# Kernel optimization log

Hardware: AMD Instinct MI355X
Metric: run time of the kernel (lower is better)

Reference implementation:

```python
import jax, jax.numpy as jnp
import numpy as np

DIM = 512
NUM_HEAD = 8
HEAD_DIM = DIM // NUM_HEAD
FFN = 4 * DIM


def setup_inputs() -> dict:
    key = jax.random.key(0)
    ks = jax.random.split(key, 16)
    s = DIM ** -0.5
    inp = {
        "x": jax.random.normal(ks[0], (4, 2048, DIM), jnp.float32),
        "wq": jax.random.normal(ks[1], (DIM, DIM), jnp.float32) * s,
        "bq": jnp.zeros((DIM,), jnp.float32),
        "wk": jax.random.normal(ks[2], (DIM, DIM), jnp.float32) * s,
        "bk": jnp.zeros((DIM,), jnp.float32),
        "wv": jax.random.normal(ks[3], (DIM, DIM), jnp.float32) * s,
        "bv": jnp.zeros((DIM,), jnp.float32),
        "wo": jax.random.normal(ks[4], (DIM, DIM), jnp.float32) * s,
        "bo": jnp.zeros((DIM,), jnp.float32),
        "w1": jax.random.normal(ks[5], (DIM, FFN), jnp.float32) * s,
        "b1": jnp.zeros((FFN,), jnp.float32),
        "w2": jax.random.normal(ks[6], (FFN, DIM), jnp.float32) * (FFN ** -0.5),
        "b2": jnp.zeros((DIM,), jnp.float32),
        "g1": jnp.ones((DIM,), jnp.float32),
        "be1": jnp.zeros((DIM,), jnp.float32),
        "g2": jnp.ones((DIM,), jnp.float32),
        "be2": jnp.zeros((DIM,), jnp.float32),
    }
    return inp


def layer_norm(x, g, b, eps=1e-5):
    mu = jnp.mean(x, axis=-1, keepdims=True)
    var = jnp.var(x, axis=-1, keepdims=True)
    return (x - mu) * jax.lax.rsqrt(var + eps) * g + b


def _forward(x, wq, bq, wk, bk, wv, bv, wo, bo, w1, b1, w2, b2, g1, be1, g2, be2):
    b, n, _ = x.shape
    scale = HEAD_DIM ** -0.5
    q = (x @ wq + bq).reshape(b, n, NUM_HEAD, HEAD_DIM).transpose(0, 2, 1, 3)
    k = (x @ wk + bk).reshape(b, n, NUM_HEAD, HEAD_DIM).transpose(0, 2, 1, 3)
    v = (x @ wv + bv).reshape(b, n, NUM_HEAD, HEAD_DIM).transpose(0, 2, 1, 3)
    scores = jnp.einsum('bhqd,bhkd->bhqk', q, k) * scale
    attn = jax.nn.softmax(scores, axis=-1)
    out = jnp.einsum('bhqk,bhkd->bhqd', attn, v)
    out = out.transpose(0, 2, 1, 3).reshape(b, n, DIM)
    out = out @ wo + bo
    x = layer_norm(out + x, g1, be1)
    h = jax.nn.gelu(x @ w1 + b1, approximate=False)
    ff = h @ w2 + b2
    x = layer_norm(ff + x, g2, be2)
    return x


def reference(x, wq, bq, wk, bk, wv, bv, wo, bo, w1, b1, w2, b2, g1, be1, g2, be2):
    return _forward(x, wq, bq, wk, bk, wv, bv, wo, bo, w1, b1, w2, b2, g1, be1, g2, be2)
```

## Files before the change

kernel.cpp:

```cpp
#include <hip/hip_runtime.h>
#include <math.h>

#define DIM 512
#define NHEAD 8
#define HD 64
#define FFN_DIM 2048
#define BATCH 4
#define SEQ 2048
#define MTOK (BATCH*SEQ)

typedef __attribute__((ext_vector_type(8))) short bf16x8;
typedef __attribute__((ext_vector_type(4))) short bf16x4;
typedef __attribute__((ext_vector_type(4))) float f32x4;
typedef __attribute__((ext_vector_type(2))) unsigned int u32x2;
typedef __attribute__((ext_vector_type(4))) unsigned int u32x4;

__device__ __forceinline__ unsigned short f2b(float f){
    unsigned int u = __float_as_uint(f);
    u += 0x7fffu + ((u >> 16) & 1u);
    return (unsigned short)(u >> 16);
}
__device__ __forceinline__ float b2f(unsigned short u){
    return __uint_as_float(((unsigned int)u) << 16);
}
__device__ __forceinline__ unsigned int pack_trunc(float f0, float f1){
    return __builtin_amdgcn_perm(__float_as_uint(f1), __float_as_uint(f0), 0x07060302u);
}
__device__ __forceinline__ void async_cp16(const unsigned short* g, unsigned short* l){
    __builtin_amdgcn_global_load_lds((const __attribute__((address_space(1))) unsigned int*)g,
                                     (__attribute__((address_space(3))) unsigned int*)l, 16, 0, 0);
}
__device__ __forceinline__ float gelu_fast(float x){
    float x3 = x*x*x;
    float y  = 2.302588f * (x + 0.044715f*x3);
    float t  = __builtin_amdgcn_exp2f(y);
    return x * t * __builtin_amdgcn_rcpf(t + 1.0f);
}

__device__ __forceinline__ void transp32(const float* __restrict__ in, unsigned short* __restrict__ out,
                                         int N, int K, int n0_rd, int n0_wr, int k0,
                                         unsigned short (&t)[32][33], int tid){
    int tx = tid & 31, ty = tid >> 5;
    #pragma unroll
    for (int u = 0; u < 4; u++)
        t[tx][ty + 8*u] = f2b(in[(size_t)(k0 + ty + 8*u)*N + n0_rd + tx]);
    __syncthreads();
    #pragma unroll
    for (int u = 0; u < 4; u++)
        out[(size_t)(n0_wr + ty + 8*u)*K + k0 + tx] = t[ty + 8*u][tx];
}

__global__ void prep_kernel(const float* __restrict__ x,
                            const float* __restrict__ wq, const float* __restrict__ wk,
                            const float* __restrict__ wv, const float* __restrict__ wo,
                            const float* __restrict__ w1, const float* __restrict__ w2,
                            const float* __restrict__ bq, const float* __restrict__ bk,
                            const float* __restrict__ bv,
                            unsigned short* __restrict__ xb, unsigned short* __restrict__ wqkvT,
                            unsigned short* __restrict__ woT, unsigned short* __restrict__ w1T,
                            unsigned short* __restrict__ w2T, float* __restrict__ bqkv)
{
    __shared__ unsigned short t[32][33];
    int bid = blockIdx.x, tid = threadIdx.x;
    if (bid < 4096) {
        int i = (bid*256 + tid)*4;
        float4 v = *(const float4*)(x + i);
        ushort4 o; o.x=f2b(v.x); o.y=f2b(v.y); o.z=f2b(v.z); o.w=f2b(v.w);
        *(ushort4*)(xb + i) = o;
    } else if (bid < 4864) {
        int r = bid - 4096;
        int n0 = (r % 48)*32, k0 = (r / 48)*32;
        const float* w = (n0 < 512) ? wq : (n0 < 1024) ? wk : wv;
        transp32(w, wqkvT, 512, 512, n0 & 511, n0, k0, t, tid);
    } else if (bid < 5120) {
        int r = bid - 4864;
        int n0 = (r % 16)*32, k0 = (r / 16)*32;
        transp32(wo, woT, 512, 512, n0, n0, k0, t, tid);
    } else if (bid < 6144) {
        int r = bid - 5120;
        int n0 = (r % 64)*32, k0 = (r / 64)*32;
        transp32(w1, w1T, 2048, 512, n0, n0, k0, t, tid);
    } else if (bid < 7168) {
        int r = bid - 6144;
        int n0 = (r % 16)*32, k0 = (r / 16)*32;
        transp32(w2, w2T, 512, 2048, n0, n0, k0, t, tid);
    } else {
        int i = (bid - 7168)*256 + tid;
        if (i < 1536)
            bqkv[i] = (i < 512) ? bq[i] : (i < 1024) ? bk[i-512] : bv[i-1024];
    }
}

template<int MODE, int SK>
__global__ __launch_bounds__(256, 4)
void gemm_bf16(const unsigned short* __restrict__ A, const unsigned short* __restrict__ Bt,
               const float* __restrict__ bias,
               unsigned short* __restrict__ Cb,
               unsigned short* __restrict__ qo, unsigned short* __restrict__ ko,
               unsigned short* __restrict__ vTo,
               int M, int N, int K)
{
    __shared__ unsigned short As[128*64];
    __shared__ unsigned short Bs[128*64];
    int tid  = threadIdx.x;
    int lane = tid & 63;
    int ln = lane & 15, qd = lane >> 4;
    int m0 = blockIdx.x * 128, n0 = blockIdx.y * 128;
    int wid = tid >> 6;
    int wm = (wid >> 1) * 64;
    int wn = (wid & 1) * 64;
    int kbeg = (SK > 1) ? (int)blockIdx.z * (K/SK) : 0;
    int kend = kbeg + K/SK;
    if (SK > 1 && MODE == 0) Cb += (size_t)blockIdx.z * M * N;

    f32x4 acc[4][4];
    #pragma unroll
    for (int i = 0; i < 4; i++)
        #pragma unroll
        for (int j = 0; j < 4; j++) acc[i][j] = (f32x4){0.f,0.f,0.f,0.f};

    for (int k0 = kbeg; k0 < kend; k0 += 64) {
        #pragma unroll
        for (int i = 0; i < 4; i++) {
            int cid = i*256 + tid;
            int row = cid >> 3, cs = cid & 7;
            int cg = cs ^ (row & 7);
            async_cp16(&A[(size_t)(m0+row)*K + k0 + cg*8], &As[(cid & ~63) * 8]);
        }
        #pragma unroll
        for (int i = 0; i < 4; i++) {
            int cid = i*256 + tid;
            int row = cid >> 3, cs = cid & 7;
            int cg = cs ^ (row & 7);
            async_cp16(&Bt[(size_t)(n0+row)*K + k0 + cg*8], &Bs[(cid & ~63) * 8]);
        }
        __syncthreads();
        #pragma unroll
        for (int kk = 0; kk < 64; kk += 32) {
            int c0 = kk >> 3;
            bf16x8 af[4], bf[4];
            #pragma unroll
            for (int t = 0; t < 4; t++)
                af[t] = *(bf16x8*)&As[(wm + t*16 + ln)*64 + ((c0 + qd) ^ (ln & 7))*8];
            #pragma unroll
            for (int t = 0; t < 4; t++)
                bf[t] = *(bf16x8*)&Bs[(wn + t*16 + ln)*64 + ((c0 + qd) ^ (ln & 7))*8];
            #pragma unroll
            for (int i = 0; i < 4; i++)
                #pragma unroll
                for (int j = 0; j < 4; j++)
                    acc[i][j] = __builtin_amdgcn_mfma_f32_16x16x32_bf16(af[i], bf[j], acc[i][j], 0,0,0);
        }
        __syncthreads();
    }

    const float QSCALE = 0.18033688011112042f;
    #pragma unroll
    for (int i = 0; i < 4; i++) {
        int mb = m0 + wm + i*16 + qd*4;
        #pragma unroll
        for (int j = 0; j < 4; j++) {
            int c = n0 + wn + j*16 + ln;
            float bv_ = (SK > 1 && blockIdx.z) ? 0.f : bias[c];
            float v[4];
            #pragma unroll
            for (int r = 0; r < 4; r++) v[r] = acc[i][j][r] + bv_;
            if (MODE == 0) {
                #pragma unroll
                for (int r = 0; r < 4; r++) Cb[(size_t)(mb+r)*N + c] = f2b(v[r]);
            } else if (MODE == 2) {
                #pragma unroll
                for (int r = 0; r < 4; r++)
                    Cb[(size_t)(mb+r)*N + c] = f2b(gelu_fast(v[r]));
            } else {
                int b = mb >> 11, t0 = mb & 2047;
                if (c < 512) {
                    int h = c >> 6, hd = c & 63;
                    #pragma unroll
                    for (int r = 0; r < 4; r++)
                        qo[(((size_t)(b*8 + h))*SEQ + t0 + r)*64 + hd] = f2b(v[r] * QSCALE);
                } else if (c < 1024) {
                    int cc = c - 512, h = cc >> 6, hd = cc & 63;
                    #pragma unroll
                    for (int r = 0; r < 4; r++)
                        ko[(((size_t)(b*8 + h))*SEQ + t0 + r)*64 + hd] = f2b(v[r]);
                } else {
                    int cc = c - 1024, h = cc >> 6, hd = cc & 63;
                    ushort4 pk;
                    pk.x = f2b(v[0]); pk.y = f2b(v[1]); pk.z = f2b(v[2]); pk.w = f2b(v[3]);
                    *(ushort4*)&vTo[(((size_t)(b*8 + h))*64 + hd)*SEQ + t0] = pk;
                }
            }
        }
    }
}

#define ATTN_BODY(KT_, KOF_, PREF_, VMC_)                                               \
  {                                                                                     \
    asm volatile("s_waitcnt vmcnt(" #VMC_ ")" ::: "memory");                            \
    __builtin_amdgcn_s_barrier();                                                       \
    __builtin_amdgcn_sched_barrier(0);                                                  \
    if (PREF_) {                                                                        \
      const int nb = (KOF_ + 16384) % 24576;                                            \
      async_cp16(&K [((size_t)bh*SEQ + ((KT_)+2)*64 + srow)*64 + scg*8], &lds[nb + sdst]); \
      async_cp16(&VT[((size_t)bh*64 + srow)*SEQ + ((KT_)+2)*64 + scg*8], &lds[nb + 4096 + sdst]); \
    }                                                                                   \
    bf16x8 kf[2][2];                                                                    \
    _Pragma("unroll")                                                                   \
    for (int ntl = 0; ntl < 2; ntl++) {                                                 \
      kf[ntl][0] = *(const bf16x8*)&kp0[(KOF_) + ntl*1024];                             \
      kf[ntl][1] = *(const bf16x8*)&kp1[(KOF_) + ntl*1024];                             \
    }                                                                                   \
    f32x4 s[2][2];                                                                      \
    _Pragma("unroll")                                                                   \
    for (int qs = 0; qs < 2; qs++)                                                      \
      _Pragma("unroll")                                                                 \
      for (int ntl = 0; ntl < 2; ntl++) s[qs][ntl] = (f32x4){0.f,0.f,0.f,0.f};          \
    __builtin_amdgcn_s_setprio(1);                                                      \
    _Pragma("unroll")                                                                   \
    for (int kk = 0; kk < 2; kk++) {                                                    \
      _Pragma("unroll")                                                                 \
      for (int ntl = 0; ntl < 2; ntl++) {                                               \
        s[0][ntl] = __builtin_amdgcn_mfma_f32_16x16x32_bf16(kf[ntl][kk], qf[0][kk], s[0][ntl], 0,0,0); \
        s[1][ntl] = __builtin_amdgcn_mfma_f32_16x16x32_bf16(kf[ntl][kk], qf[1][kk], s[1][ntl], 0,0,0); \
      }                                                                                 \
    }                                                                                   \
    __builtin_amdgcn_s_setprio(0);                                                      \
    bf16x8 pf[2];                                                                       \
    _Pragma("unroll")                                                                   \
    for (int qs = 0; qs < 2; qs++) {                                                    \
      float p[8];                                                                       \
      _Pragma("unroll")                                                                 \
      for (int ntl = 0; ntl < 2; ntl++)                                                 \
        _Pragma("unroll")                                                               \
        for (int r = 0; r < 4; r++) p[ntl*4+r] = __builtin_amdgcn_exp2f(s[qs][ntl][r]); \
      l_i[qs] += ((p[0]+p[1])+(p[2]+p[3])) + ((p[4]+p[5])+(p[6]+p[7]));                 \
      u32x4 pu;                                                                         \
      pu[0] = pack_trunc(p[0], p[1]); pu[1] = pack_trunc(p[2], p[3]);                   \
      pu[2] = pack_trunc(p[4], p[5]); pu[3] = pack_trunc(p[6], p[7]);                   \
      pf[qs] = __builtin_bit_cast(bf16x8, pu);                                          \
    }                                                                                   \
    __builtin_amdgcn_s_setprio(1);                                                      \
    _Pragma("unroll")                                                                   \
    for (int dt = 0; dt < 4; dt++) {                                                    \
      u32x2 va = *(const u32x2*)&vpA[(KOF_) + 4096 + dt*1024];                          \
      u32x2 vb = *(const u32x2*)&vpB[(KOF_) + 4096 + dt*1024];                          \
      u32x4 vv; vv[0] = va[0]; vv[1] = va[1]; vv[2] = vb[0]; vv[3] = vb[1];             \
      bf16x8 vf = __builtin_bit_cast(bf16x8, vv);                                       \
      o[0][dt] = __builtin_amdgcn_mfma_f32_16x16x32_bf16(vf, pf[0], o[0][dt], 0,0,0);   \
      o[1][dt] = __builtin_amdgcn_mfma_f32_16x16x32_bf16(vf, pf[1], o[1][dt], 0,0,0);   \
    }                                                                                   \
    __builtin_amdgcn_s_setprio(0);                                                      \
  }

__global__ __launch_bounds__(512, 2)
void attn_mfma(const unsigned short* __restrict__ Q, const unsigned short* __restrict__ K,
               const unsigned short* __restrict__ VT, unsigned short* __restrict__ O)
{
    __shared__ unsigned short lds[24576];
    int tid  = threadIdx.x;
    int wid  = tid >> 6, lane = tid & 63;
    int ln = lane & 15, qd = lane >> 4;
    int wq = wid & 3;
    int wk = wid >> 2;
    int bx = blockIdx.x;
    int qb = (bx >> 3) & 15;
    int bh = (bx & 7) + 8 * (bx >> 7);

    bf16x8 qf[2][2];
    #pragma unroll
    for (int qs = 0; qs < 2; qs++)
        #pragma unroll
        for (int kk = 0; kk < 2; kk++)
            qf[qs][kk] = *(const bf16x8*)&Q[((size_t)bh*SEQ + qb*128 + wq*32 + qs*16 + ln)*64 + kk*32 + qd*8];

    int srow = tid >> 3, scs = tid & 7, scg = scs ^ (srow & 7);
    int sdst = (tid & ~63) * 8;
    #pragma unroll
    for (int t = 0; t < 2; t++) {
        async_cp16(&K [((size_t)bh*SEQ + t*64 + srow)*64 + scg*8], &lds[t*8192 + sdst]);
        async_cp16(&VT[((size_t)bh*64 + srow)*SEQ + t*64 + scg*8], &lds[t*8192 + 4096 + sdst]);
    }

    const unsigned short* kp0 = lds + wk*2048 + ln*64 + ((0*4 + qd) ^ (ln & 7))*8;
    const unsigned short* kp1 = lds + wk*2048 + ln*64 + ((1*4 + qd) ^ (ln & 7))*8;
    const unsigned short* vpA = lds + ln*64 + ((wk*4     + (qd>>1)) ^ (ln & 7))*8 + (qd & 1)*4;
    const unsigned short* vpB = lds + ln*64 + ((wk*4 + 2 + (qd>>1)) ^ (ln & 7))*8 + (qd & 1)*4;

    f32x4 o[2][4];
    #pragma unroll
    for (int qs = 0; qs < 2; qs++)
        #pragma unroll
        for (int dt = 0; dt < 4; dt++) o[qs][dt] = (f32x4){0.f,0.f,0.f,0.f};
    float l_i[2] = {0.f, 0.f};

    for (int kt3 = 0; kt3 < 30; kt3 += 3) {
        ATTN_BODY(kt3 + 0, 0,     true, 2)
        ATTN_BODY(kt3 + 1, 8192,  true, 2)
        ATTN_BODY(kt3 + 2, 16384, true, 2)
    }
    ATTN_BODY(30, 0,    false, 2)
    ATTN_BODY(31, 8192, false, 0)

    float l[2];
    #pragma unroll
    for (int qs = 0; qs < 2; qs++) {
        float t = l_i[qs];
        t += __shfl_xor(t, 16);
        t += __shfl_xor(t, 32);
        l[qs] = t;
    }

    __syncthreads();
    float* fl = (float*)lds;
    if (wk == 1) {
        #pragma unroll
        for (int qs = 0; qs < 2; qs++) {
            #pragma unroll
            for (int dt = 0; dt < 4; dt++)
                *(f32x4*)&fl[(((wq*2 + qs)*4 + dt)*64 + lane)*4] = o[qs][dt];
            fl[8192 + (wq*2 + qs)*64 + lane] = l[qs];
        }
    }
    __syncthreads();
    if (wk == 0) {
        int b = bh >> 3, h = bh & 7;
        #pragma unroll
        for (int qs = 0; qs < 2; qs++) {
            float lt = l[qs] + fl[8192 + (wq*2 + qs)*64 + lane];
            float linv = 1.0f / lt;
            int t = qb*128 + wq*32 + qs*16 + ln;
            #pragma unroll
            for (int dt = 0; dt < 4; dt++) {
                f32x4 po = *(f32x4*)&fl[(((wq*2 + qs)*4 + dt)*64 + lane)*4];
                ushort4 pk;
                pk.x = f2b((o[qs][dt][0] + po[0])*linv);
                pk.y = f2b((o[qs][dt][1] + po[1])*linv);
                pk.z = f2b((o[qs][dt][2] + po[2])*linv);
                pk.w = f2b((o[qs][dt][3] + po[3])*linv);
                *(ushort4*)&O[((size_t)b*SEQ + t)*DIM + h*64 + dt*16 + qd*4] = pk;
            }
        }
    }
}

__global__ void ln1_kernel(const unsigned short* __restrict__ m0b, const unsigned short* __restrict__ m1b,
                           const float* __restrict__ resp,
                           const float* __restrict__ g, const float* __restrict__ be,
                           unsigned short* __restrict__ outb)
{
    int row  = blockIdx.x*4 + (threadIdx.x >> 6);
    int lane = threadIdx.x & 63;
    size_t base = (size_t)row * DIM + lane*8;

    ushort4 a0 = *(const ushort4*)(m0b + base);
    ushort4 a1 = *(const ushort4*)(m0b + base + 4);
    ushort4 c0 = *(const ushort4*)(m1b + base);
    ushort4 c1 = *(const ushort4*)(m1b + base + 4);
    float4 r0 = *(const float4*)(resp + base);
    float4 r1 = *(const float4*)(resp + base + 4);
    float v[8] = { b2f(a0.x)+b2f(c0.x)+r0.x, b2f(a0.y)+b2f(c0.y)+r0.y,
                   b2f(a0.z)+b2f(c0.z)+r0.z, b2f(a0.w)+b2f(c0.w)+r0.w,
                   b2f(a1.x)+b2f(c1.x)+r1.x, b2f(a1.y)+b2f(c1.y)+r1.y,
                   b2f(a1.z)+b2f(c1.z)+r1.z, b2f(a1.w)+b2f(c1.w)+r1.w };
    float s = 0.f, s2 = 0.f;
    #pragma unroll
    for (int i = 0; i < 8; i++) { s += v[i]; s2 += v[i]*v[i]; }
    #pragma unroll
    for (int d = 32; d >= 1; d >>= 1) { s += __shfl_xor(s, d); s2 += __shfl_xor(s2, d); }
    float mean = s * (1.0f / DIM);
    float rstd = rsqrtf(s2 * (1.0f / DIM) - mean*mean + 1e-5f);

    float4 g0 = *(const float4*)(g + lane*8);
    float4 g1 = *(const float4*)(g + lane*8 + 4);
    float4 b0 = *(const float4*)(be + lane*8);
    float4 b1 = *(const float4*)(be + lane*8 + 4);
    float gg[8] = {g0.x,g0.y,g0.z,g0.w,g1.x,g1.y,g1.z,g1.w};
    float bb[8] = {b0.x,b0.y,b0.z,b0.w,b1.x,b1.y,b1.z,b1.w};
    float o[8];
    #pragma unroll
    for (int i = 0; i < 8; i++) o[i] = (v[i]-mean)*rstd*gg[i] + bb[i];
    ushort4 p0, p1;
    p0.x=f2b(o[0]); p0.y=f2b(o[1]); p0.z=f2b(o[2]); p0.w=f2b(o[3]);
    p1.x=f2b(o[4]); p1.y=f2b(o[5]); p1.z=f2b(o[6]); p1.w=f2b(o[7]);
    *(ushort4*)(outb + base)     = p0;
    *(ushort4*)(outb + base + 4) = p1;
}

__global__ void ln2_kernel(const unsigned short* __restrict__ m0b, const unsigned short* __restrict__ m1b,
                           const unsigned short* __restrict__ resb,
                           const float* __restrict__ g, const float* __restrict__ be,
                           float* __restrict__ outf)
{
    int row  = blockIdx.x*4 + (threadIdx.x >> 6);
    int lane = threadIdx.x & 63;
    size_t base = (size_t)row * DIM + lane*8;

    ushort4 a0 = *(const ushort4*)(m0b + base);
    ushort4 a1 = *(const ushort4*)(m0b + base + 4);
    ushort4 c0 = *(const ushort4*)(m1b + base);
    ushort4 c1 = *(const ushort4*)(m1b + base + 4);
    ushort4 rb0 = *(const ushort4*)(resb + base);
    ushort4 rb1 = *(const ushort4*)(resb + base + 4);
    float v[8] = { b2f(a0.x)+b2f(c0.x)+b2f(rb0.x), b2f(a0.y)+b2f(c0.y)+b2f(rb0.y),
                   b2f(a0.z)+b2f(c0.z)+b2f(rb0.z), b2f(a0.w)+b2f(c0.w)+b2f(rb0.w),
                   b2f(a1.x)+b2f(c1.x)+b2f(rb1.x), b2f(a1.y)+b2f(c1.y)+b2f(rb1.y),
                   b2f(a1.z)+b2f(c1.z)+b2f(rb1.z), b2f(a1.w)+b2f(c1.w)+b2f(rb1.w) };
    float s = 0.f, s2 = 0.f;
    #pragma unroll
    for (int i = 0; i < 8; i++) { s += v[i]; s2 += v[i]*v[i]; }
    #pragma unroll
    for (int d = 32; d >= 1; d >>= 1) { s += __shfl_xor(s, d); s2 += __shfl_xor(s2, d); }
    float mean = s * (1.0f / DIM);
    float rstd = rsqrtf(s2 * (1.0f / DIM) - mean*mean + 1e-5f);

    float4 g0 = *(const float4*)(g + lane*8);
    float4 g1 = *(const float4*)(g + lane*8 + 4);
    float4 b0 = *(const float4*)(be + lane*8);
    float4 b1 = *(const float4*)(be + lane*8 + 4);
    float gg[8] = {g0.x,g0.y,g0.z,g0.w,g1.x,g1.y,g1.z,g1.w};
    float bb[8] = {b0.x,b0.y,b0.z,b0.w,b1.x,b1.y,b1.z,b1.w};
    float o[8];
    #pragma unroll
    for (int i = 0; i < 8; i++) o[i] = (v[i] - mean)*rstd*gg[i] + bb[i];
    *(float4*)(outf + base)     = (float4){o[0],o[1],o[2],o[3]};
    *(float4*)(outf + base + 4) = (float4){o[4],o[5],o[6],o[7]};
}

extern "C" void kernel_launch(void* const* d_in, const int* in_sizes, int n_in,
                              void* d_out, int out_size, void* d_ws, size_t ws_size,
                              hipStream_t stream) {
    const float* x   = (const float*)d_in[0];
    const float* wq  = (const float*)d_in[1];
    const float* bq  = (const float*)d_in[2];
    const float* wk  = (const float*)d_in[3];
    const float* bk  = (const float*)d_in[4];
    const float* wv  = (const float*)d_in[5];
    const float* bv  = (const float*)d_in[6];
    const float* wo  = (const float*)d_in[7];
    const float* bo  = (const float*)d_in[8];
    const float* w1  = (const float*)d_in[9];
    const float* b1  = (const float*)d_in[10];
    const float* w2  = (const float*)d_in[11];
    const float* b2  = (const float*)d_in[12];
    const float* g1  = (const float*)d_in[13];
    const float* be1 = (const float*)d_in[14];
    const float* g2  = (const float*)d_in[15];
    const float* be2 = (const float*)d_in[16];
    float* out = (float*)d_out;

    char* w = (char*)d_ws;
    size_t off = 0;
    auto alloc = [&](size_t bytes){ void* p = w + off; off += (bytes + 255) & ~(size_t)255; return p; };
    unsigned short* xb     = (unsigned short*)alloc((size_t)MTOK*DIM*2);
    unsigned short* wqkvT  = (unsigned short*)alloc((size_t)1536*512*2);
    unsigned short* woT    = (unsigned short*)alloc((size_t)512*512*2);
    unsigned short* w1T    = (unsigned short*)alloc((size_t)2048*512*2);
    unsigned short* w2T    = (unsigned short*)alloc((size_t)512*2048*2);
    float*          bqkv   = (float*)alloc(1536*4);
    unsigned short* qb_    = (unsigned short*)alloc((size_t)32*SEQ*64*2);
    unsigned short* kb_    = (unsigned short*)alloc((size_t)32*SEQ*64*2);
    unsigned short* vT_    = (unsigned short*)alloc((size_t)32*64*SEQ*2);
    unsigned short* attno  = (unsigned short*)alloc((size_t)MTOK*DIM*2);
    unsigned short* x1b    = (unsigned short*)alloc((size_t)MTOK*DIM*2);
    unsigned short* h_     = (unsigned short*)alloc((size_t)MTOK*FFN_DIM*2);
    unsigned short* ffb    = (unsigned short*)alloc((size_t)2*MTOK*DIM*2);

    prep_kernel<<<7174, 256, 0, stream>>>(x, wq, wk, wv, wo, w1, w2, bq, bk, bv,
                                          xb, wqkvT, woT, w1T, w2T, bqkv);

    gemm_bf16<1,1><<<dim3(64,12), 256, 0, stream>>>(xb, wqkvT, bqkv, nullptr,
                                                    qb_, kb_, vT_, MTOK, 1536, DIM);
    attn_mfma<<<512, 512, 0, stream>>>(qb_, kb_, vT_, attno);
    gemm_bf16<0,2><<<dim3(64,4,2), 256, 0, stream>>>(attno, woT, bo, ffb,
                                                     nullptr, nullptr, nullptr, MTOK, DIM, DIM);
    ln1_kernel<<<MTOK/4, 256, 0, stream>>>(ffb, ffb + (size_t)MTOK*DIM, x, g1, be1, x1b);
    gemm_bf16<2,1><<<dim3(64,16), 256, 0, stream>>>(x1b, w1T, b1, h_,
                                                    nullptr, nullptr, nullptr, MTOK, FFN_DIM, DIM);
    gemm_bf16<0,2><<<dim3(64,4,2), 256, 0, stream>>>(h_, w2T, b2, ffb,
                                                     nullptr, nullptr, nullptr, MTOK, DIM, FFN_DIM);
    ln2_kernel<<<MTOK/4, 256, 0, stream>>>(ffb, ffb + (size_t)MTOK*DIM, x1b, g2, be2, out);
}
```

Baseline: 237.5 us.

## Double-buffer GEMM LDS tiles with async prefetch and MFMA priority

Doubles the GEMM shared-memory allocation into two stages and prefetches the next K-tile with async copies while the current tile is consumed, using explicit vmcnt waits and barriers in place of __syncthreads. It also raises wave priority around the MFMA block. The aim is to hide global-load latency behind matrix math. In exchange, LDS use per block doubles to 64KB, which can cut occupancy below the launch-bounds target of 4 blocks. The loop also assumes an even number of K-tiles.

```diff
diff --git a/kernel.cpp b/kernel.cpp
--- a/kernel.cpp
+++ b/kernel.cpp
@@ -100,8 +100,7 @@
                unsigned short* __restrict__ vTo,
                int M, int N, int K)
 {
-    __shared__ unsigned short As[128*64];
-    __shared__ unsigned short Bs[128*64];
+    __shared__ unsigned short lds[32768];
     int tid  = threadIdx.x;
     int lane = tid & 63;
     int ln = lane & 15, qd = lane >> 4;
@@ -110,7 +109,7 @@
     int wm = (wid >> 1) * 64;
     int wn = (wid & 1) * 64;
     int kbeg = (SK > 1) ? (int)blockIdx.z * (K/SK) : 0;
-    int kend = kbeg + K/SK;
+    int nk = (K/SK) >> 6;
     if (SK > 1 && MODE == 0) Cb += (size_t)blockIdx.z * M * N;
 
     f32x4 acc[4][4];
@@ -119,40 +118,68 @@
         #pragma unroll
         for (int j = 0; j < 4; j++) acc[i][j] = (f32x4){0.f,0.f,0.f,0.f};
 
-    for (int k0 = kbeg; k0 < kend; k0 += 64) {
-        #pragma unroll
-        for (int i = 0; i < 4; i++) {
-            int cid = i*256 + tid;
-            int row = cid >> 3, cs = cid & 7;
-            int cg = cs ^ (row & 7);
-            async_cp16(&A[(size_t)(m0+row)*K + k0 + cg*8], &As[(cid & ~63) * 8]);
+#define G_STAGE(K0_, BUF_)                                                              \
+    {                                                                                   \
+        _Pragma("unroll")                                                               \
+        for (int i = 0; i < 4; i++) {                                                   \
+            int cid = i*256 + tid;                                                      \
+            int row = cid >> 3, cs = cid & 7;                                           \
+            int cg = cs ^ (row & 7);                                                    \
+            async_cp16(&A[(size_t)(m0+row)*K + (K0_) + cg*8], &lds[(BUF_) + (cid & ~63) * 8]); \
+        }                                                                               \
+        _Pragma("unroll")                                                               \
+        for (int i = 0; i < 4; i++) {                                                   \
+            int cid = i*256 + tid;                                                      \
+            int row = cid >> 3, cs = cid & 7;                                           \
+            int cg = cs ^ (row & 7);                                                    \
+            async_cp16(&Bt[(size_t)(n0+row)*K + (K0_) + cg*8], &lds[(BUF_) + 8192 + (cid & ~63) * 8]); \
+        }                                                                               \
+    }
+
+#define G_COMPUTE(BUF_)                                                                 \
+    {                                                                                   \
+        _Pragma("unroll")                                                               \
+        for (int kk = 0; kk < 64; kk += 32) {                                           \
+            int c0 = kk >> 3;                                                           \
+            bf16x8 af[4], bf[4];                                                        \
+            _Pragma("unroll")                                                           \
+            for (int t = 0; t < 4; t++)                                                 \
+                af[t] = *(bf16x8*)&lds[(BUF_) + (wm + t*16 + ln)*64 + ((c0 + qd) ^ (ln & 7))*8]; \
+            _Pragma("unroll")                                                           \
+            for (int t = 0; t < 4; t++)                                                 \
+                bf[t] = *(bf16x8*)&lds[(BUF_) + 8192 + (wn + t*16 + ln)*64 + ((c0 + qd) ^ (ln & 7))*8]; \
+            __builtin_amdgcn_s_setprio(1);                                              \
+            _Pragma("unroll")                                                           \
+            for (int i = 0; i < 4; i++)                                                 \
+                _Pragma("unroll")                                                       \
+                for (int j = 0; j < 4; j++)                                             \
+                    acc[i][j] = __builtin_amdgcn_mfma_f32_16x16x32_bf16(af[i], bf[j], acc[i][j], 0,0,0); \
+            __builtin_amdgcn_s_setprio(0);                                              \
+        }                                                                               \
+    }
+
+    G_STAGE(kbeg, 0)
+
+    for (int kp = 0; kp < nk; kp += 2) {
+        G_STAGE(kbeg + (kp+1)*64, 16384)
+        asm volatile("s_waitcnt vmcnt(8)" ::: "memory");
+        __builtin_amdgcn_s_barrier();
+        G_COMPUTE(0)
+        asm volatile("s_waitcnt lgkmcnt(0)" ::: "memory");
+        __builtin_amdgcn_s_barrier();
+        if (kp + 2 < nk) {
+            G_STAGE(kbeg + (kp+2)*64, 0)
+            asm volatile("s_waitcnt vmcnt(8)" ::: "memory");
+        } else {
+            asm volatile("s_waitcnt vmcnt(0)" ::: "memory");
         }
-        #pragma unroll
-        for (int i = 0; i < 4; i++) {
-            int cid = i*256 + tid;
-            int row = cid >> 3, cs = cid & 7;
-            int cg = cs ^ (row & 7);
-            async_cp16(&Bt[(size_t)(n0+row)*K + k0 + cg*8], &Bs[(cid & ~63) * 8]);
-        }
-        __syncthreads();
-        #pragma unroll
-        for (int kk = 0; kk < 64; kk += 32) {
-            int c0 = kk >> 3;
-            bf16x8 af[4], bf[4];
-            #pragma unroll
-            for (int t = 0; t < 4; t++)
-                af[t] = *(bf16x8*)&As[(wm + t*16 + ln)*64 + ((c0 + qd) ^ (ln & 7))*8];
-            #pragma unroll
-            for (int t = 0; t < 4; t++)
-                bf[t] = *(bf16x8*)&Bs[(wn + t*16 + ln)*64 + ((c0 + qd) ^ (ln & 7))*8];
-            #pragma unroll
-            for (int i = 0; i < 4; i++)
-                #pragma unroll
-                for (int j = 0; j < 4; j++)
-                    acc[i][j] = __builtin_amdgcn_mfma_f32_16x16x32_bf16(af[i], bf[j], acc[i][j], 0,0,0);
-        }
-        __syncthreads();
-    }
+        __builtin_amdgcn_s_barrier();
+        G_COMPUTE(16384)
+        asm volatile("s_waitcnt lgkmcnt(0)" ::: "memory");
+        __builtin_amdgcn_s_barrier();
+    }
+#undef G_STAGE
+#undef G_COMPUTE
 
     const float QSCALE = 0.18033688011112042f;
     #pragma unroll
```

After: 238.3 us. About the same (+0.3%).

## Triple-buffer GEMM K-loop with async prefetch and single barrier per step

Applied to the files above, without the earlier changes.

Replaces the single-buffered 64-wide K tile GEMM loop with a three-stage ring of 32-wide K tiles in shared memory. Loads for tile t+2 are issued while tile t is computed, waiting with vmcnt counts instead of full syncs, with one barrier per step and raised wave priority around the MFMA block. The swizzle is adapted to 32-element rows. Shared memory grows to 48KB, so launch bounds drop to 3 blocks per CU, which may reduce occupancy.

```diff
diff --git a/kernel.cpp b/kernel.cpp
--- a/kernel.cpp
+++ b/kernel.cpp
@@ -92,7 +92,7 @@
 }
 
 template<int MODE, int SK>
-__global__ __launch_bounds__(256, 4)
+__global__ __launch_bounds__(256, 3)
 void gemm_bf16(const unsigned short* __restrict__ A, const unsigned short* __restrict__ Bt,
                const float* __restrict__ bias,
                unsigned short* __restrict__ Cb,
@@ -100,8 +100,7 @@
                unsigned short* __restrict__ vTo,
                int M, int N, int K)
 {
-    __shared__ unsigned short As[128*64];
-    __shared__ unsigned short Bs[128*64];
+    __shared__ unsigned short lds[24576];
     int tid  = threadIdx.x;
     int lane = tid & 63;
     int ln = lane & 15, qd = lane >> 4;
@@ -110,7 +109,7 @@
     int wm = (wid >> 1) * 64;
     int wn = (wid & 1) * 64;
     int kbeg = (SK > 1) ? (int)blockIdx.z * (K/SK) : 0;
-    int kend = kbeg + K/SK;
+    int nk = (K/SK) >> 5;
     if (SK > 1 && MODE == 0) Cb += (size_t)blockIdx.z * M * N;
 
     f32x4 acc[4][4];
@@ -119,40 +118,57 @@
         #pragma unroll
         for (int j = 0; j < 4; j++) acc[i][j] = (f32x4){0.f,0.f,0.f,0.f};
 
-    for (int k0 = kbeg; k0 < kend; k0 += 64) {
-        #pragma unroll
-        for (int i = 0; i < 4; i++) {
-            int cid = i*256 + tid;
-            int row = cid >> 3, cs = cid & 7;
-            int cg = cs ^ (row & 7);
-            async_cp16(&A[(size_t)(m0+row)*K + k0 + cg*8], &As[(cid & ~63) * 8]);
+#define G_STAGE(K0_, BUF_)                                                              \
+    {                                                                                   \
+        _Pragma("unroll")                                                               \
+        for (int i = 0; i < 2; i++) {                                                   \
+            int cid = i*256 + tid;                                                      \
+            int row = cid >> 2, cs = cid & 3;                                           \
+            int cg = cs ^ ((row >> 1) & 3);                                             \
+            async_cp16(&A[(size_t)(m0+row)*K + (K0_) + cg*8], &lds[(BUF_) + (cid & ~63) * 8]); \
+        }                                                                               \
+        _Pragma("unroll")                                                               \
+        for (int i = 0; i < 2; i++) {                                                   \
+            int cid = i*256 + tid;                                                      \
+            int row = cid >> 2, cs = cid & 3;                                           \
+            int cg = cs ^ ((row >> 1) & 3);                                             \
+            async_cp16(&Bt[(size_t)(n0+row)*K + (K0_) + cg*8], &lds[(BUF_) + 4096 + (cid & ~63) * 8]); \
+        }                                                                               \
+    }
+
+    G_STAGE(kbeg,      0)
+    G_STAGE(kbeg + 32, 8192)
+
+    int swz = (qd ^ ((ln >> 1) & 3)) * 8;
+    int aoff = (wm + ln)*32 + swz;
+    int boff = 4096 + (wn + ln)*32 + swz;
+
+    int kof = 0;
+    for (int t = 0; t < nk; t++) {
+        if (t < nk - 1) { asm volatile("s_waitcnt vmcnt(4)" ::: "memory"); }
+        else            { asm volatile("s_waitcnt vmcnt(0)" ::: "memory"); }
+        __builtin_amdgcn_s_barrier();
+        __builtin_amdgcn_sched_barrier(0);
+        if (t < nk - 2) {
+            int nb = kof + 16384; if (nb >= 24576) nb -= 24576;
+            G_STAGE(kbeg + (t+2)*32, nb)
         }
-        #pragma unroll
-        for (int i = 0; i < 4; i++) {
-            int cid = i*256 + tid;
-            int row = cid >> 3, cs = cid & 7;
-            int cg = cs ^ (row & 7);
-            async_cp16(&Bt[(size_t)(n0+row)*K + k0 + cg*8], &Bs[(cid & ~63) * 8]);
+        bf16x8 af[4], bf[4];
+        #pragma unroll
+        for (int tt = 0; tt < 4; tt++) {
+            af[tt] = *(bf16x8*)&lds[kof + aoff + tt*512];
+            bf[tt] = *(bf16x8*)&lds[kof + boff + tt*512];
         }
-        __syncthreads();
-        #pragma unroll
-        for (int kk = 0; kk < 64; kk += 32) {
-            int c0 = kk >> 3;
-            bf16x8 af[4], bf[4];
+        __builtin_amdgcn_s_setprio(1);
+        #pragma unroll
+        for (int i = 0; i < 4; i++)
             #pragma unroll
-            for (int t = 0; t < 4; t++)
-                af[t] = *(bf16x8*)&As[(wm + t*16 + ln)*64 + ((c0 + qd) ^ (ln & 7))*8];
-            #pragma unroll
-            for (int t = 0; t < 4; t++)
-                bf[t] = *(bf16x8*)&Bs[(wn + t*16 + ln)*64 + ((c0 + qd) ^ (ln & 7))*8];
-            #pragma unroll
-            for (int i = 0; i < 4; i++)
-                #pragma unroll
-                for (int j = 0; j < 4; j++)
-                    acc[i][j] = __builtin_amdgcn_mfma_f32_16x16x32_bf16(af[i], bf[j], acc[i][j], 0,0,0);
-        }
-        __syncthreads();
-    }
+            for (int j = 0; j < 4; j++)
+                acc[i][j] = __builtin_amdgcn_mfma_f32_16x16x32_bf16(af[i], bf[j], acc[i][j], 0,0,0);
+        __builtin_amdgcn_s_setprio(0);
+        kof += 8192; if (kof >= 24576) kof = 0;
+    }
+#undef G_STAGE
 
     const float QSCALE = 0.18033688011112042f;
     #pragma unroll
```

Result: no change. 238.6 us (+0.5%).
